# Optimization experiments

Hardware: AMD Instinct MI355X
Metric: run time of the kernel (lower is better)

Reference implementation:

```python
import jax, jax.numpy as jnp
import numpy as np

WS = 7           # window side
N = WS * WS      # tokens per window = 49
DIM = 384
H = 12
HD = DIM // H    # 32
BW = 2048        # num_windows * batch
NW = 4           # windows per image (mask batch)
SCALE = 1.0 / float(np.sqrt(HD))


def _rel_index():
    coords = np.stack(np.meshgrid(np.arange(WS), np.arange(WS), indexing='ij'))  # (2,7,7)
    flat = coords.reshape(2, -1)                      # (2,49)
    rel = flat[:, :, None] - flat[:, None, :]         # (2,49,49)
    rel = rel.transpose(1, 2, 0).copy()               # (49,49,2)
    rel[..., 0] += WS - 1
    rel[..., 1] += WS - 1
    rel[..., 0] *= 2 * WS - 1
    return jnp.asarray(rel.sum(-1), dtype=jnp.int32)  # (49,49)


def setup_inputs() -> dict:
    key = jax.random.key(0)
    ks = jax.random.split(key, 16)
    f32 = jnp.float32
    se = jax.random.normal(ks[0], (BW, N, DIM), dtype=f32)
    de = jax.random.normal(ks[1], (BW, N, DIM), dtype=f32)
    mask = jnp.where(jax.random.uniform(ks[2], (NW, N, N)) < 0.1, f32(-1e9), f32(0.0))
    s = 0.02
    w_v_se = jax.random.normal(ks[3], (DIM, DIM), dtype=f32) * s
    b_v_se = jnp.zeros((DIM,), dtype=f32)
    w_qkv = jax.random.normal(ks[4], (3 * DIM, DIM), dtype=f32) * s
    b_qkv = jnp.zeros((3 * DIM,), dtype=f32)
    w_proj_se = jax.random.normal(ks[5], (DIM, DIM), dtype=f32) * s
    b_proj_se = jnp.zeros((DIM,), dtype=f32)
    w_proj_de = jax.random.normal(ks[6], (DIM, DIM), dtype=f32) * s
    b_proj_de = jnp.zeros((DIM,), dtype=f32)
    rpb = jax.random.normal(ks[7], ((2 * WS - 1) ** 2, H), dtype=f32) * s  # (169,12)
    rel_idx = _rel_index()
    return {
        'se': se, 'de': de, 'mask': mask,
        'w_v_se': w_v_se, 'b_v_se': b_v_se,
        'w_qkv': w_qkv, 'b_qkv': b_qkv,
        'w_proj_se': w_proj_se, 'b_proj_se': b_proj_se,
        'w_proj_de': w_proj_de, 'b_proj_de': b_proj_de,
        'rpb': rpb, 'rel_idx': rel_idx,
    }


def reference(se, de, mask, w_v_se, b_v_se, w_qkv, b_qkv,
              w_proj_se, b_proj_se, w_proj_de, b_proj_de, rpb, rel_idx):
    B_, N_, C = se.shape
    # qkv from de (coa=False branch)
    qkv = (de @ w_qkv.T + b_qkv).reshape(B_, N_, 3, H, HD).transpose(2, 0, 3, 1, 4)
    q, k, v_de = qkv[0], qkv[1], qkv[2]                 # (B_,H,N,HD)
    v_se = (se @ w_v_se.T + b_v_se).reshape(B_, N_, H, HD).transpose(0, 2, 1, 3)
    attn = jnp.einsum('bhnd,bhmd->bhnm', q * SCALE, k)  # (B_,H,N,N)
    bias = rpb[rel_idx].transpose(2, 0, 1)              # (H,N,N)
    attn = attn + bias[None]
    # add window mask: view as (B, nW, H, N, N)
    attn = attn.reshape(B_ // NW, NW, H, N_, N_) + mask[None, :, None]
    attn = jax.nn.softmax(attn.reshape(B_, H, N_, N_), axis=-1)
    se_o = jnp.einsum('bhnm,bhmd->bnhd', attn, v_se).reshape(B_, N_, C)
    de_o = jnp.einsum('bhnm,bhmd->bnhd', attn, v_de).reshape(B_, N_, C)
    se_o = se_o @ w_proj_se.T + b_proj_se
    de_o = de_o @ w_proj_de.T + b_proj_de
    return (se_o, de_o)
```

## Files before the change

### kernel.cpp

```cpp
#include <hip/hip_runtime.h>

typedef _Float16 f16;
typedef __attribute__((ext_vector_type(8))) _Float16 f16x8;
typedef __attribute__((ext_vector_type(4))) _Float16 f16x4;
typedef __attribute__((ext_vector_type(4))) float f32x4;

#define MFMA16(a, b, c) __builtin_amdgcn_mfma_f32_16x16x32_f16(a, b, c, 0, 0, 0)

#define SCALE_F 0.17677669529663687f
#define NHEAD 12
#define NTOK 49
#define NBW 2048

__global__ void cast_f32_to_f16(const float* __restrict__ in, f16* __restrict__ out, int n4) {
    int i0 = blockIdx.x * 256 + threadIdx.x;
    int stride = gridDim.x * 256;
    for (int i = i0; i < n4; i += stride) {
        f32x4 v = ((const f32x4*)in)[i];
        f16x4 o;
#pragma unroll
        for (int e = 0; e < 4; ++e) o[e] = (f16)v[e];
        ((f16x4*)out)[i] = o;
    }
}

__global__ void prep_bm(const float* __restrict__ rpb, const int* __restrict__ rel_idx,
                        const float* __restrict__ mask, float* __restrict__ bm) {
    int blk = blockIdx.x;
    int w4 = blk / NHEAD, h = blk - w4 * NHEAD;
    for (int idx = threadIdx.x; idx < 4096; idx += 64) {
        int r = idx >> 6, c = idx & 63;
        float v = -1e30f;
        if (r < NTOK && c < NTOK)
            v = rpb[rel_idx[r * NTOK + c] * NHEAD + h] + mask[(w4 * NTOK + r) * NTOK + c];
        bm[(size_t)blk * 4096 + idx] = v;
    }
}

template <typename OUT_T>
__global__ __launch_bounds__(256) void gemm_bt(const f16* __restrict__ A, const f16* __restrict__ B,
                                               const float* __restrict__ bias, OUT_T* __restrict__ C,
                                               int M, int N, int K) {
    __shared__ __align__(16) f16 As[128 * 64];
    __shared__ __align__(16) f16 Bs[128 * 64];
    const int nwg = gridDim.x * gridDim.y;
    int wg = blockIdx.y * gridDim.x + blockIdx.x;
    wg = (wg & 7) * (nwg >> 3) + (wg >> 3);
    const int m0 = (wg / gridDim.x) * 128, n0 = (wg % gridDim.x) * 128;
    const int tid = threadIdx.x;
    const int w = tid >> 6, l = tid & 63;
    const int wm = w >> 1, wn = w & 1;
    const int lr = l & 15, lg = l >> 4;
    const int sp = l & 7;

    f32x4 acc[4][4] = {};

    for (int k0 = 0; k0 < K; k0 += 64) {
        __syncthreads();
#pragma unroll
        for (int it = 0; it < 4; ++it) {
            int row = w * 32 + it * 8 + (l >> 3);
            int gchunk = sp ^ (row & 7);
            const f16* gA = A + (size_t)(m0 + row) * K + k0 + gchunk * 8;
            const f16* gB = B + (size_t)(n0 + row) * K + k0 + gchunk * 8;
            f16* lA = As + (w * 32 + it * 8) * 64;
            f16* lB = Bs + (w * 32 + it * 8) * 64;
            __builtin_amdgcn_global_load_lds((const __attribute__((address_space(1))) void*)gA,
                                             (__attribute__((address_space(3))) void*)lA, 16, 0, 0);
            __builtin_amdgcn_global_load_lds((const __attribute__((address_space(1))) void*)gB,
                                             (__attribute__((address_space(3))) void*)lB, 16, 0, 0);
        }
        __syncthreads();
#pragma unroll
        for (int ks = 0; ks < 2; ++ks) {
            f16x8 af[4], bfr[4];
#pragma unroll
            for (int mi = 0; mi < 4; ++mi) {
                int r = 64 * wm + 16 * mi + lr;
                int chunk = (lg + 4 * ks) ^ (r & 7);
                af[mi] = *(const f16x8*)(As + r * 64 + chunk * 8);
            }
#pragma unroll
            for (int ni = 0; ni < 4; ++ni) {
                int r = 64 * wn + 16 * ni + lr;
                int chunk = (lg + 4 * ks) ^ (r & 7);
                bfr[ni] = *(const f16x8*)(Bs + r * 64 + chunk * 8);
            }
#pragma unroll
            for (int mi = 0; mi < 4; ++mi)
#pragma unroll
                for (int ni = 0; ni < 4; ++ni)
                    acc[mi][ni] = MFMA16(af[mi], bfr[ni], acc[mi][ni]);
        }
    }
#pragma unroll
    for (int mi = 0; mi < 4; ++mi) {
#pragma unroll
        for (int ni = 0; ni < 4; ++ni) {
            int col = n0 + 64 * wn + 16 * ni + lr;
            float bv = bias[col];
#pragma unroll
            for (int reg = 0; reg < 4; ++reg) {
                int row = m0 + 64 * wm + 16 * mi + 4 * lg + reg;
                C[(size_t)row * N + col] = (OUT_T)(acc[mi][ni][reg] + bv);
            }
        }
    }
}

__global__ __launch_bounds__(64) void attn_kernel(const f16* __restrict__ qkv,
                                                  const f16* __restrict__ vse,
                                                  const float* __restrict__ bm_all,
                                                  f16* __restrict__ att_se, f16* __restrict__ att_de) {
    __shared__ __align__(16) f16 Ps[64 * 64];

    const int bh = blockIdx.x;
    const int b = bh / NHEAD, h = bh - b * NHEAD;
    const int l = threadIdx.x;
    const int lr = l & 15, lg = l >> 4;
    const size_t wbase = (size_t)b * NTOK;

    f16x8 qa[4], kb[4];
#pragma unroll
    for (int mi = 0; mi < 4; ++mi)
        qa[mi] = *(const f16x8*)(qkv + (wbase + 16 * mi + lr) * 1152 + h * 32 + lg * 8);
#pragma unroll
    for (int ni = 0; ni < 4; ++ni)
        kb[ni] = *(const f16x8*)(qkv + (wbase + 16 * ni + lr) * 1152 + 384 + h * 32 + lg * 8);

    const f32x4 zero4 = {0.f, 0.f, 0.f, 0.f};
    f32x4 S[4][4];
    __builtin_amdgcn_s_setprio(1);
#pragma unroll
    for (int mi = 0; mi < 4; ++mi)
#pragma unroll
        for (int ni = 0; ni < 4; ++ni)
            S[mi][ni] = MFMA16(qa[mi], kb[ni], zero4);
    __builtin_amdgcn_s_setprio(0);

    const float* bmp = bm_all + (size_t)((b & 3) * NHEAD + h) * 4096;
#pragma unroll
    for (int mi = 0; mi < 4; ++mi) {
#pragma unroll
        for (int reg = 0; reg < 4; ++reg) {
            int r = 16 * mi + 4 * lg + reg;
            float v[4];
#pragma unroll
            for (int ni = 0; ni < 4; ++ni)
                v[ni] = S[mi][ni][reg] * SCALE_F + bmp[(r << 6) + 16 * ni + lr];
            float mx = fmaxf(fmaxf(v[0], v[1]), fmaxf(v[2], v[3]));
#pragma unroll
            for (int off = 1; off < 16; off <<= 1) mx = fmaxf(mx, __shfl_xor(mx, off));
            float e[4];
            float sm = 0.f;
#pragma unroll
            for (int ni = 0; ni < 4; ++ni) {
                e[ni] = __expf(v[ni] - mx);
                sm += e[ni];
            }
#pragma unroll
            for (int off = 1; off < 16; off <<= 1) sm += __shfl_xor(sm, off);
            float inv = 1.f / sm;
#pragma unroll
            for (int ni = 0; ni < 4; ++ni)
                Ps[(r << 6) + ((16 * ni + lr) ^ ((r & 7) << 3))] = (f16)(e[ni] * inv);
        }
    }
    __syncthreads();

#pragma unroll
    for (int s = 0; s < 2; ++s) {
        const f16* vbase = s ? (qkv + wbase * 1152 + 768 + h * 32) : (vse + wbase * 384 + h * 32);
        const int RS = s ? 1152 : 384;
        f32x4 o[4][2] = {};
#pragma unroll
        for (int ks = 0; ks < 2; ++ks) {
            f16x8 pa[4];
#pragma unroll
            for (int mi = 0; mi < 4; ++mi) {
                int r = 16 * mi + lr;
                pa[mi] = *(const f16x8*)(Ps + (r << 6) + ((8 * lg + 32 * ks) ^ ((r & 7) << 3)));
            }
#pragma unroll
            for (int ni = 0; ni < 2; ++ni) {
                const f16* p = vbase + (size_t)(8 * lg + 32 * ks) * RS + 16 * ni + lr;
                f16x8 vb;
#pragma unroll
                for (int e = 0; e < 8; ++e) vb[e] = p[(size_t)e * RS];
                __builtin_amdgcn_s_setprio(1);
#pragma unroll
                for (int mi = 0; mi < 4; ++mi) o[mi][ni] = MFMA16(pa[mi], vb, o[mi][ni]);
                __builtin_amdgcn_s_setprio(0);
            }
        }
        f16* dst = s ? att_de : att_se;
#pragma unroll
        for (int mi = 0; mi < 4; ++mi) {
#pragma unroll
            for (int reg = 0; reg < 4; ++reg) {
                int r = 16 * mi + 4 * lg + reg;
                if (r < NTOK) {
#pragma unroll
                    for (int ni = 0; ni < 2; ++ni)
                        dst[(wbase + r) * 384 + h * 32 + 16 * ni + lr] = (f16)o[mi][ni][reg];
                }
            }
        }
    }
}

extern "C" void kernel_launch(void* const* d_in, const int* in_sizes, int n_in,
                              void* d_out, int out_size, void* d_ws, size_t ws_size,
                              hipStream_t stream) {
    const float* se = (const float*)d_in[0];
    const float* de = (const float*)d_in[1];
    const float* mask = (const float*)d_in[2];
    const float* w_v_se = (const float*)d_in[3];
    const float* b_v_se = (const float*)d_in[4];
    const float* w_qkv = (const float*)d_in[5];
    const float* b_qkv = (const float*)d_in[6];
    const float* w_proj_se = (const float*)d_in[7];
    const float* b_proj_se = (const float*)d_in[8];
    const float* w_proj_de = (const float*)d_in[9];
    const float* b_proj_de = (const float*)d_in[10];
    const float* rpb = (const float*)d_in[11];
    const int* rel_idx = (const int*)d_in[12];

    const size_t SE_ELEMS = (size_t)NBW * NTOK * 384;

    char* ws = (char*)d_ws;
    f16* de_h = (f16*)(ws);
    f16* se_h = (f16*)(ws + 77070336);
    f16* qkv_h = (f16*)(ws + 154140672);
    f16* vse_h = (f16*)(ws + 385351680);
    f16* wqkv_h = (f16*)(ws + 462422016);
    f16* wvse_h = (f16*)(ws + 463306752);
    f16* wpse_h = (f16*)(ws + 463601664);
    f16* wpde_h = (f16*)(ws + 463896576);
    float* bm = (float*)(ws + 464191488);

    auto cast = [&](const float* in, f16* out, size_t n) {
        int n4 = (int)(n / 4);
        int blocks = (n4 + 255) / 256;
        if (blocks > 2048) blocks = 2048;
        cast_f32_to_f16<<<blocks, 256, 0, stream>>>(in, out, n4);
    };
    cast(de, de_h, SE_ELEMS);
    cast(se, se_h, SE_ELEMS);
    cast(w_qkv, wqkv_h, (size_t)1152 * 384);
    cast(w_v_se, wvse_h, (size_t)384 * 384);
    cast(w_proj_se, wpse_h, (size_t)384 * 384);
    cast(w_proj_de, wpde_h, (size_t)384 * 384);

    prep_bm<<<48, 64, 0, stream>>>(rpb, rel_idx, mask, bm);

    gemm_bt<f16><<<dim3(9, 784), 256, 0, stream>>>(de_h, wqkv_h, b_qkv, qkv_h, 100352, 1152, 384);
    gemm_bt<f16><<<dim3(3, 784), 256, 0, stream>>>(se_h, wvse_h, b_v_se, vse_h, 100352, 384, 384);

    attn_kernel<<<NBW * NHEAD, 64, 0, stream>>>(qkv_h, vse_h, bm, de_h, se_h);

    gemm_bt<float><<<dim3(3, 784), 256, 0, stream>>>(de_h, wpse_h, b_proj_se, (float*)d_out, 100352, 384, 384);
    gemm_bt<float><<<dim3(3, 784), 256, 0, stream>>>(se_h, wpde_h, b_proj_de, (float*)d_out + SE_ELEMS, 100352,
                                                     384, 384);
}
```

Before: 681.8 us.

## Fuse fp32-to-fp16 input casts into GEMM tile loads and prefetch V fragments

The QKV and V_se projection GEMMs now read fp32 activations directly, convert them in registers and store swizzled fp16 tiles into LDS, so the two standalone cast kernels over the large inputs are removed. This drops a full write and reread of the activations in fp16. In exchange, the A tiles are loaded synchronously through registers instead of as async global-to-LDS copies, and the fp32 data is reread once per column tile. The attention kernel also issues its strided V loads before the softmax so their latency overlaps with that computation, at the cost of more registers.

```diff
diff --git a/kernel.cpp b/kernel.cpp
--- a/kernel.cpp
+++ b/kernel.cpp
@@ -37,8 +37,8 @@
     }
 }
 
-template <typename OUT_T>
-__global__ __launch_bounds__(256) void gemm_bt(const f16* __restrict__ A, const f16* __restrict__ B,
+template <typename OUT_T, bool A_F32>
+__global__ __launch_bounds__(256) void gemm_bt(const void* __restrict__ Av, const f16* __restrict__ B,
                                                const float* __restrict__ bias, OUT_T* __restrict__ C,
                                                int M, int N, int K) {
     __shared__ __align__(16) f16 As[128 * 64];
@@ -57,18 +57,51 @@
 
     for (int k0 = 0; k0 < K; k0 += 64) {
         __syncthreads();
-#pragma unroll
-        for (int it = 0; it < 4; ++it) {
-            int row = w * 32 + it * 8 + (l >> 3);
-            int gchunk = sp ^ (row & 7);
-            const f16* gA = A + (size_t)(m0 + row) * K + k0 + gchunk * 8;
-            const f16* gB = B + (size_t)(n0 + row) * K + k0 + gchunk * 8;
-            f16* lA = As + (w * 32 + it * 8) * 64;
-            f16* lB = Bs + (w * 32 + it * 8) * 64;
-            __builtin_amdgcn_global_load_lds((const __attribute__((address_space(1))) void*)gA,
-                                             (__attribute__((address_space(3))) void*)lA, 16, 0, 0);
-            __builtin_amdgcn_global_load_lds((const __attribute__((address_space(1))) void*)gB,
-                                             (__attribute__((address_space(3))) void*)lB, 16, 0, 0);
+        if constexpr (A_F32) {
+            const float* A32 = (const float*)Av;
+            f32x4 t0[4], t1[4];
+#pragma unroll
+            for (int it = 0; it < 4; ++it) {
+                int row = w * 32 + it * 8 + (l >> 3);
+                const float* g = A32 + (size_t)(m0 + row) * K + k0 + sp * 8;
+                t0[it] = *(const f32x4*)g;
+                t1[it] = *(const f32x4*)(g + 4);
+            }
+#pragma unroll
+            for (int it = 0; it < 4; ++it) {
+                int row = w * 32 + it * 8 + (l >> 3);
+                f16x8 hx;
+#pragma unroll
+                for (int e = 0; e < 4; ++e) {
+                    hx[e] = (f16)t0[it][e];
+                    hx[e + 4] = (f16)t1[it][e];
+                }
+                *(f16x8*)(As + row * 64 + (sp ^ (row & 7)) * 8) = hx;
+            }
+#pragma unroll
+            for (int it = 0; it < 4; ++it) {
+                int row = w * 32 + it * 8 + (l >> 3);
+                int gchunk = sp ^ (row & 7);
+                const f16* gB = B + (size_t)(n0 + row) * K + k0 + gchunk * 8;
+                f16* lB = Bs + (w * 32 + it * 8) * 64;
+                __builtin_amdgcn_global_load_lds((const __attribute__((address_space(1))) void*)gB,
+                                                 (__attribute__((address_space(3))) void*)lB, 16, 0, 0);
+            }
+        } else {
+            const f16* A16 = (const f16*)Av;
+#pragma unroll
+            for (int it = 0; it < 4; ++it) {
+                int row = w * 32 + it * 8 + (l >> 3);
+                int gchunk = sp ^ (row & 7);
+                const f16* gA = A16 + (size_t)(m0 + row) * K + k0 + gchunk * 8;
+                const f16* gB = B + (size_t)(n0 + row) * K + k0 + gchunk * 8;
+                f16* lA = As + (w * 32 + it * 8) * 64;
+                f16* lB = Bs + (w * 32 + it * 8) * 64;
+                __builtin_amdgcn_global_load_lds((const __attribute__((address_space(1))) void*)gA,
+                                                 (__attribute__((address_space(3))) void*)lA, 16, 0, 0);
+                __builtin_amdgcn_global_load_lds((const __attribute__((address_space(1))) void*)gB,
+                                                 (__attribute__((address_space(3))) void*)lB, 16, 0, 0);
+            }
         }
         __syncthreads();
 #pragma unroll
@@ -138,6 +171,21 @@
             S[mi][ni] = MFMA16(qa[mi], kb[ni], zero4);
     __builtin_amdgcn_s_setprio(0);
 
+    f16x8 vbr[2][2][2];
+#pragma unroll
+    for (int s = 0; s < 2; ++s) {
+        const f16* vbase = s ? (qkv + wbase * 1152 + 768 + h * 32) : (vse + wbase * 384 + h * 32);
+        const int RS = s ? 1152 : 384;
+#pragma unroll
+        for (int ks = 0; ks < 2; ++ks)
+#pragma unroll
+            for (int ni = 0; ni < 2; ++ni) {
+                const f16* p = vbase + (size_t)(8 * lg + 32 * ks) * RS + 16 * ni + lr;
+#pragma unroll
+                for (int e = 0; e < 8; ++e) vbr[s][ks][ni][e] = p[(size_t)e * RS];
+            }
+    }
+
     const float* bmp = bm_all + (size_t)((b & 3) * NHEAD + h) * 4096;
 #pragma unroll
     for (int mi = 0; mi < 4; ++mi) {
@@ -170,8 +218,6 @@
 
 #pragma unroll
     for (int s = 0; s < 2; ++s) {
-        const f16* vbase = s ? (qkv + wbase * 1152 + 768 + h * 32) : (vse + wbase * 384 + h * 32);
-        const int RS = s ? 1152 : 384;
         f32x4 o[4][2] = {};
 #pragma unroll
         for (int ks = 0; ks < 2; ++ks) {
@@ -181,17 +227,12 @@
                 int r = 16 * mi + lr;
                 pa[mi] = *(const f16x8*)(Ps + (r << 6) + ((8 * lg + 32 * ks) ^ ((r & 7) << 3)));
             }
-#pragma unroll
-            for (int ni = 0; ni < 2; ++ni) {
-                const f16* p = vbase + (size_t)(8 * lg + 32 * ks) * RS + 16 * ni + lr;
-                f16x8 vb;
-#pragma unroll
-                for (int e = 0; e < 8; ++e) vb[e] = p[(size_t)e * RS];
-                __builtin_amdgcn_s_setprio(1);
-#pragma unroll
-                for (int mi = 0; mi < 4; ++mi) o[mi][ni] = MFMA16(pa[mi], vb, o[mi][ni]);
-                __builtin_amdgcn_s_setprio(0);
-            }
+            __builtin_amdgcn_s_setprio(1);
+#pragma unroll
+            for (int ni = 0; ni < 2; ++ni)
+#pragma unroll
+                for (int mi = 0; mi < 4; ++mi) o[mi][ni] = MFMA16(pa[mi], vbr[s][ks][ni], o[mi][ni]);
+            __builtin_amdgcn_s_setprio(0);
         }
         f16* dst = s ? att_de : att_se;
 #pragma unroll
@@ -229,8 +270,8 @@
     const size_t SE_ELEMS = (size_t)NBW * NTOK * 384;
 
     char* ws = (char*)d_ws;
-    f16* de_h = (f16*)(ws);
-    f16* se_h = (f16*)(ws + 77070336);
+    f16* att_se = (f16*)(ws);
+    f16* att_de = (f16*)(ws + 77070336);
     f16* qkv_h = (f16*)(ws + 154140672);
     f16* vse_h = (f16*)(ws + 385351680);
     f16* wqkv_h = (f16*)(ws + 462422016);
@@ -245,8 +286,6 @@
         if (blocks > 2048) blocks = 2048;
         cast_f32_to_f16<<<blocks, 256, 0, stream>>>(in, out, n4);
     };
-    cast(de, de_h, SE_ELEMS);
-    cast(se, se_h, SE_ELEMS);
     cast(w_qkv, wqkv_h, (size_t)1152 * 384);
     cast(w_v_se, wvse_h, (size_t)384 * 384);
     cast(w_proj_se, wpse_h, (size_t)384 * 384);
@@ -254,12 +293,13 @@
 
     prep_bm<<<48, 64, 0, stream>>>(rpb, rel_idx, mask, bm);
 
-    gemm_bt<f16><<<dim3(9, 784), 256, 0, stream>>>(de_h, wqkv_h, b_qkv, qkv_h, 100352, 1152, 384);
-    gemm_bt<f16><<<dim3(3, 784), 256, 0, stream>>>(se_h, wvse_h, b_v_se, vse_h, 100352, 384, 384);
-
-    attn_kernel<<<NBW * NHEAD, 64, 0, stream>>>(qkv_h, vse_h, bm, de_h, se_h);
-
-    gemm_bt<float><<<dim3(3, 784), 256, 0, stream>>>(de_h, wpse_h, b_proj_se, (float*)d_out, 100352, 384, 384);
-    gemm_bt<float><<<dim3(3, 784), 256, 0, stream>>>(se_h, wpde_h, b_proj_de, (float*)d_out + SE_ELEMS, 100352,
-                                                     384, 384);
-}
+    gemm_bt<f16, true><<<dim3(9, 784), 256, 0, stream>>>((const void*)de, wqkv_h, b_qkv, qkv_h, 100352, 1152, 384);
+    gemm_bt<f16, true><<<dim3(3, 784), 256, 0, stream>>>((const void*)se, wvse_h, b_v_se, vse_h, 100352, 384, 384);
+
+    attn_kernel<<<NBW * NHEAD, 64, 0, stream>>>(qkv_h, vse_h, bm, att_se, att_de);
+
+    gemm_bt<float, false><<<dim3(3, 784), 256, 0, stream>>>((const void*)att_se, wpse_h, b_proj_se, (float*)d_out,
+                                                            100352, 384, 384);
+    gemm_bt<float, false><<<dim3(3, 784), 256, 0, stream>>>((const void*)att_de, wpde_h, b_proj_de,
+                                                            (float*)d_out + SE_ELEMS, 100352, 384, 384);
+}
```

After: 613.8 us. 1.11x faster.

## Replace GEMMs with 256x256 double-buffered 8-wave kernel and hoist attention V loads

Applied to the files above, without the earlier changes.

Replaces the 128x128 single-buffered GEMM with a 512-thread kernel that computes 256x256 tiles. Its K loop is hardcoded to 384 and fully unrolled. Loads go through double-buffered LDS staging, and the async global-to-LDS copies are interleaved with MFMA groups under explicit vmcnt waits and barriers, so memory latency is meant to overlap with compute. Because N is padded up to multiples of 256, the kernel does extra MFMA work (most on the N=384 GEMMs) and reads weight rows past the end of each weight buffer; only the stores are guarded. In the attention kernel, the strided V fragment loads are moved ahead of the softmax so they overlap with it, which costs more registers.

```diff
diff --git a/kernel.cpp b/kernel.cpp
--- a/kernel.cpp
+++ b/kernel.cpp
@@ -11,6 +11,13 @@
 #define NHEAD 12
 #define NTOK 49
 #define NBW 2048
+
+#define SB() __builtin_amdgcn_s_barrier()
+#define SCHEDB() __builtin_amdgcn_sched_barrier(0)
+#define WAITV4() asm volatile("s_waitcnt vmcnt(4)" ::: "memory")
+#define WAITV0() asm volatile("s_waitcnt vmcnt(0)" ::: "memory")
+#define WAITV8() asm volatile("s_waitcnt vmcnt(8)" ::: "memory")
+#define WAITL0() asm volatile("s_waitcnt lgkmcnt(0)" ::: "memory")
 
 __global__ void cast_f32_to_f16(const float* __restrict__ in, f16* __restrict__ out, int n4) {
     int i0 = blockIdx.x * 256 + threadIdx.x;
@@ -38,71 +45,150 @@
 }
 
 template <typename OUT_T>
-__global__ __launch_bounds__(256) void gemm_bt(const f16* __restrict__ A, const f16* __restrict__ B,
-                                               const float* __restrict__ bias, OUT_T* __restrict__ C,
-                                               int M, int N, int K) {
-    __shared__ __align__(16) f16 As[128 * 64];
-    __shared__ __align__(16) f16 Bs[128 * 64];
+__global__ __launch_bounds__(512, 2) void gemm8(const f16* __restrict__ A, const f16* __restrict__ B,
+                                                const float* __restrict__ bias, OUT_T* __restrict__ C,
+                                                int Nreal, int ldc) {
+    __shared__ __align__(16) f16 LA[2][256][64];
+    __shared__ __align__(16) f16 LB[2][256][64];
+
     const int nwg = gridDim.x * gridDim.y;
     int wg = blockIdx.y * gridDim.x + blockIdx.x;
     wg = (wg & 7) * (nwg >> 3) + (wg >> 3);
-    const int m0 = (wg / gridDim.x) * 128, n0 = (wg % gridDim.x) * 128;
+    const int m0 = (wg / gridDim.x) * 256;
+    const int n0 = (wg % gridDim.x) * 256;
+
     const int tid = threadIdx.x;
     const int w = tid >> 6, l = tid & 63;
-    const int wm = w >> 1, wn = w & 1;
+    const int wm = w >> 2, wn = w & 3;
     const int lr = l & 15, lg = l >> 4;
-    const int sp = l & 7;
-
-    f32x4 acc[4][4] = {};
-
-    for (int k0 = 0; k0 < K; k0 += 64) {
-        __syncthreads();
-#pragma unroll
-        for (int it = 0; it < 4; ++it) {
-            int row = w * 32 + it * 8 + (l >> 3);
-            int gchunk = sp ^ (row & 7);
-            const f16* gA = A + (size_t)(m0 + row) * K + k0 + gchunk * 8;
-            const f16* gB = B + (size_t)(n0 + row) * K + k0 + gchunk * 8;
-            f16* lA = As + (w * 32 + it * 8) * 64;
-            f16* lB = Bs + (w * 32 + it * 8) * 64;
-            __builtin_amdgcn_global_load_lds((const __attribute__((address_space(1))) void*)gA,
-                                             (__attribute__((address_space(3))) void*)lA, 16, 0, 0);
-            __builtin_amdgcn_global_load_lds((const __attribute__((address_space(1))) void*)gB,
-                                             (__attribute__((address_space(3))) void*)lB, 16, 0, 0);
-        }
-        __syncthreads();
-#pragma unroll
-        for (int ks = 0; ks < 2; ++ks) {
-            f16x8 af[4], bfr[4];
-#pragma unroll
-            for (int mi = 0; mi < 4; ++mi) {
-                int r = 64 * wm + 16 * mi + lr;
-                int chunk = (lg + 4 * ks) ^ (r & 7);
-                af[mi] = *(const f16x8*)(As + r * 64 + chunk * 8);
-            }
-#pragma unroll
-            for (int ni = 0; ni < 4; ++ni) {
-                int r = 64 * wn + 16 * ni + lr;
-                int chunk = (lg + 4 * ks) ^ (r & 7);
-                bfr[ni] = *(const f16x8*)(Bs + r * 64 + chunk * 8);
-            }
-#pragma unroll
-            for (int mi = 0; mi < 4; ++mi)
-#pragma unroll
-                for (int ni = 0; ni < 4; ++ni)
-                    acc[mi][ni] = MFMA16(af[mi], bfr[ni], acc[mi][ni]);
-        }
-    }
-#pragma unroll
-    for (int mi = 0; mi < 4; ++mi) {
+
+    const int smat = (w >= 4);
+    const int srow_base = (w & 3) * 64;
+    const int lrow = l >> 3;
+    const int lchunk = l & 7;
+
+    auto STAGE = [&](int kt, int j0) {
+#pragma unroll
+        for (int jj = 0; jj < 2; ++jj) {
+            int row0 = srow_base + (j0 + jj) * 8;
+            int r = row0 + lrow;
+            int c = lchunk ^ (r & 7);
+            const f16* src;
+            f16* dst;
+            if (smat == 0) {
+                src = A + (size_t)(m0 + r) * 384 + kt * 64 + c * 8;
+                dst = &LA[kt & 1][row0][0];
+            } else {
+                src = B + (size_t)(n0 + r) * 384 + kt * 64 + c * 8;
+                dst = &LB[kt & 1][row0][0];
+            }
+            __builtin_amdgcn_global_load_lds((const __attribute__((address_space(1))) void*)src,
+                                             (__attribute__((address_space(3))) void*)dst, 16, 0, 0);
+        }
+    };
+
+    auto LDAf = [&](int d, int mi, int ks) {
+        int r = wm * 128 + mi * 16 + lr;
+        int c = (ks * 4 + lg) ^ (r & 7);
+        return *(const f16x8*)&LA[d][r][c * 8];
+    };
+    auto LDBf = [&](int d, int ni, int ks) {
+        int r = wn * 64 + ni * 16 + lr;
+        int c = (ks * 4 + lg) ^ (r & 7);
+        return *(const f16x8*)&LB[d][r][c * 8];
+    };
+
+    f32x4 acc[8][4] = {};
+    f16x8 a[8][2], b[4][2];
+
+    STAGE(0, 0); STAGE(0, 2); STAGE(0, 4); STAGE(0, 6);
+    STAGE(1, 0); STAGE(1, 2); STAGE(1, 4); STAGE(1, 6);
+    WAITV8();
+    SB();
+    SCHEDB();
+
+    auto half_iter = [&](int D, int sekt, bool sec, int smkt, bool smc, int wv) {
+#pragma unroll
+        for (int mi = 0; mi < 4; ++mi) { a[mi][0] = LDAf(D, mi, 0); a[mi][1] = LDAf(D, mi, 1); }
+#pragma unroll
+        for (int ni = 0; ni < 2; ++ni) { b[ni][0] = LDBf(D, ni, 0); b[ni][1] = LDBf(D, ni, 1); }
+        if (sec) STAGE(sekt, 4);
+        SB();
+        __builtin_amdgcn_s_setprio(1);
+#pragma unroll
+        for (int mi = 0; mi < 4; ++mi)
+#pragma unroll
+            for (int ni = 0; ni < 2; ++ni) {
+                acc[mi][ni] = MFMA16(a[mi][0], b[ni][0], acc[mi][ni]);
+                acc[mi][ni] = MFMA16(a[mi][1], b[ni][1], acc[mi][ni]);
+            }
+        __builtin_amdgcn_s_setprio(0);
+        SB();
+#pragma unroll
+        for (int mi = 4; mi < 8; ++mi) { a[mi][0] = LDAf(D, mi, 0); a[mi][1] = LDAf(D, mi, 1); }
+#pragma unroll
+        for (int ni = 2; ni < 4; ++ni) { b[ni][0] = LDBf(D, ni, 0); b[ni][1] = LDBf(D, ni, 1); }
+        if (sec) STAGE(sekt, 6);
+        SB();
+        __builtin_amdgcn_s_setprio(1);
+#pragma unroll
+        for (int mi = 0; mi < 4; ++mi)
+#pragma unroll
+            for (int ni = 2; ni < 4; ++ni) {
+                acc[mi][ni] = MFMA16(a[mi][0], b[ni][0], acc[mi][ni]);
+                acc[mi][ni] = MFMA16(a[mi][1], b[ni][1], acc[mi][ni]);
+            }
+        __builtin_amdgcn_s_setprio(0);
+        WAITL0();
+        SB();
+        if (smc) STAGE(smkt, 0);
+        SB();
+        __builtin_amdgcn_s_setprio(1);
+#pragma unroll
+        for (int mi = 4; mi < 8; ++mi)
+#pragma unroll
+            for (int ni = 0; ni < 2; ++ni) {
+                acc[mi][ni] = MFMA16(a[mi][0], b[ni][0], acc[mi][ni]);
+                acc[mi][ni] = MFMA16(a[mi][1], b[ni][1], acc[mi][ni]);
+            }
+        __builtin_amdgcn_s_setprio(0);
+        SB();
+        if (smc) STAGE(smkt, 2);
+        SB();
+        __builtin_amdgcn_s_setprio(1);
+#pragma unroll
+        for (int mi = 4; mi < 8; ++mi)
+#pragma unroll
+            for (int ni = 2; ni < 4; ++ni) {
+                acc[mi][ni] = MFMA16(a[mi][0], b[ni][0], acc[mi][ni]);
+                acc[mi][ni] = MFMA16(a[mi][1], b[ni][1], acc[mi][ni]);
+            }
+        __builtin_amdgcn_s_setprio(0);
+        if (wv == 4) WAITV4();
+        else if (wv == 0) WAITV0();
+        SB();
+        SCHEDB();
+    };
+
+#pragma unroll
+    for (int t = 0; t < 3; ++t) {
+        const int kt0 = 2 * t, kt1 = 2 * t + 1;
+        half_iter(0, kt1, t > 0, kt0 + 2, kt0 + 2 < 6, (t < 2) ? 4 : 0);
+        half_iter(1, kt0 + 2, kt0 + 2 < 6, kt1 + 2, kt1 + 2 < 6, (t < 2) ? 4 : -1);
+    }
+
+#pragma unroll
+    for (int mi = 0; mi < 8; ++mi) {
 #pragma unroll
         for (int ni = 0; ni < 4; ++ni) {
-            int col = n0 + 64 * wn + 16 * ni + lr;
-            float bv = bias[col];
-#pragma unroll
-            for (int reg = 0; reg < 4; ++reg) {
-                int row = m0 + 64 * wm + 16 * mi + 4 * lg + reg;
-                C[(size_t)row * N + col] = (OUT_T)(acc[mi][ni][reg] + bv);
+            int col = n0 + wn * 64 + ni * 16 + lr;
+            if (col < Nreal) {
+                float bv = bias[col];
+#pragma unroll
+                for (int reg = 0; reg < 4; ++reg) {
+                    int row = m0 + wm * 128 + mi * 16 + lg * 4 + reg;
+                    C[(size_t)row * ldc + col] = (OUT_T)(acc[mi][ni][reg] + bv);
+                }
             }
         }
     }
@@ -138,6 +224,21 @@
             S[mi][ni] = MFMA16(qa[mi], kb[ni], zero4);
     __builtin_amdgcn_s_setprio(0);
 
+    f16x8 vbr[2][2][2];
+#pragma unroll
+    for (int s = 0; s < 2; ++s) {
+        const f16* vbase = s ? (qkv + wbase * 1152 + 768 + h * 32) : (vse + wbase * 384 + h * 32);
+        const int RS = s ? 1152 : 384;
+#pragma unroll
+        for (int ks = 0; ks < 2; ++ks)
+#pragma unroll
+            for (int ni = 0; ni < 2; ++ni) {
+                const f16* p = vbase + (size_t)(8 * lg + 32 * ks) * RS + 16 * ni + lr;
+#pragma unroll
+                for (int e = 0; e < 8; ++e) vbr[s][ks][ni][e] = p[(size_t)e * RS];
+            }
+    }
+
     const float* bmp = bm_all + (size_t)((b & 3) * NHEAD + h) * 4096;
 #pragma unroll
     for (int mi = 0; mi < 4; ++mi) {
@@ -170,8 +271,6 @@
 
 #pragma unroll
     for (int s = 0; s < 2; ++s) {
-        const f16* vbase = s ? (qkv + wbase * 1152 + 768 + h * 32) : (vse + wbase * 384 + h * 32);
-        const int RS = s ? 1152 : 384;
         f32x4 o[4][2] = {};
 #pragma unroll
         for (int ks = 0; ks < 2; ++ks) {
@@ -181,17 +280,12 @@
                 int r = 16 * mi + lr;
                 pa[mi] = *(const f16x8*)(Ps + (r << 6) + ((8 * lg + 32 * ks) ^ ((r & 7) << 3)));
             }
-#pragma unroll
-            for (int ni = 0; ni < 2; ++ni) {
-                const f16* p = vbase + (size_t)(8 * lg + 32 * ks) * RS + 16 * ni + lr;
-                f16x8 vb;
-#pragma unroll
-                for (int e = 0; e < 8; ++e) vb[e] = p[(size_t)e * RS];
-                __builtin_amdgcn_s_setprio(1);
-#pragma unroll
-                for (int mi = 0; mi < 4; ++mi) o[mi][ni] = MFMA16(pa[mi], vb, o[mi][ni]);
-                __builtin_amdgcn_s_setprio(0);
-            }
+            __builtin_amdgcn_s_setprio(1);
+#pragma unroll
+            for (int ni = 0; ni < 2; ++ni)
+#pragma unroll
+                for (int mi = 0; mi < 4; ++mi) o[mi][ni] = MFMA16(pa[mi], vbr[s][ks][ni], o[mi][ni]);
+            __builtin_amdgcn_s_setprio(0);
         }
         f16* dst = s ? att_de : att_se;
 #pragma unroll
@@ -254,12 +348,11 @@
 
     prep_bm<<<48, 64, 0, stream>>>(rpb, rel_idx, mask, bm);
 
-    gemm_bt<f16><<<dim3(9, 784), 256, 0, stream>>>(de_h, wqkv_h, b_qkv, qkv_h, 100352, 1152, 384);
-    gemm_bt<f16><<<dim3(3, 784), 256, 0, stream>>>(se_h, wvse_h, b_v_se, vse_h, 100352, 384, 384);
+    gemm8<f16><<<dim3(5, 392), 512, 0, stream>>>(de_h, wqkv_h, b_qkv, qkv_h, 1152, 1152);
+    gemm8<f16><<<dim3(2, 392), 512, 0, stream>>>(se_h, wvse_h, b_v_se, vse_h, 384, 384);
 
     attn_kernel<<<NBW * NHEAD, 64, 0, stream>>>(qkv_h, vse_h, bm, de_h, se_h);
 
-    gemm_bt<float><<<dim3(3, 784), 256, 0, stream>>>(de_h, wpse_h, b_proj_se, (float*)d_out, 100352, 384, 384);
-    gemm_bt<float><<<dim3(3, 784), 256, 0, stream>>>(se_h, wpde_h, b_proj_de, (float*)d_out + SE_ELEMS, 100352,
-                                                     384, 384);
-}
+    gemm8<float><<<dim3(2, 392), 512, 0, stream>>>(de_h, wpse_h, b_proj_se, (float*)d_out, 384, 384);
+    gemm8<float><<<dim3(2, 392), 512, 0, stream>>>(se_h, wpde_h, b_proj_de, (float*)d_out + SE_ELEMS, 384, 384);
+}
```

Result: slower. 737.3 us (+8.1%).
